# Kernel tuning notes

Measured on AMD Instinct MI355X. Metric: run time of the kernel, lower is better.

Reference implementation:

```python
import jax, jax.numpy as jnp
import numpy as np

M = 12      # max_context_size
H = 768     # hidden_size
NH = 8      # global encoder heads
HD = H // NH
FF = 2048   # global encoder ff_dim
B = 8192


def _gather_hist(buf, mask, idx, ctx):
    """Age-sorted gather of valid circular-buffer slots (oldest first), padded to ctx."""
    Bb, Mx, Hh = buf.shape
    pos = jnp.arange(Mx)
    age = (idx[:, None] - pos[None, :]) % Mx              # [B,M] age of each slot
    key = jnp.where(mask, -age, Mx + 1)                   # valid slots first, oldest (max age) first
    order = jnp.argsort(key, axis=1)                      # stable sort, matches python sorted()
    sorted_buf = jnp.take_along_axis(buf, order[:, :, None], axis=1)
    nvalid = mask.sum(axis=1)                             # [B]
    hist = sorted_buf[:, :ctx]                            # [B,ctx,H]
    valid = jnp.arange(ctx)[None, :] < nvalid[:, None]
    hist = hist * valid[:, :, None]                       # zero out padding rows
    return hist, jnp.minimum(nvalid, ctx)


def _seq_with_current(buf, mask, idx, z_k, ctx):
    """History (ctx-1 slots) + current utterance at the last position (faithful to original,
    including the original's padding-mask behavior arange >= hist_len+1)."""
    Bb = z_k.shape[0]
    hist, hlen = _gather_hist(buf, mask, idx, ctx - 1)
    seq = jnp.concatenate([hist, jnp.zeros((Bb, 1, buf.shape[-1]), buf.dtype)], axis=1)
    seq = seq.at[:, ctx - 1].set(z_k)
    lengths = jnp.minimum(hlen + 1, ctx)
    pad = jnp.arange(ctx)[None, :] >= lengths[:, None]    # True = padded
    return seq, lengths, pad


def _layernorm(x, g, b):
    mu = x.mean(-1, keepdims=True)
    var = x.var(-1, keepdims=True)
    return (x - mu) * jax.lax.rsqrt(var + 1e-5) * g + b


def _forward(z_k, context_buffer, buffer_mask, buffer_indices,
             Wq, bq, Wk, bk, Wv, bv, Wo, bo, ln1_g, ln1_b,
             W1, b1, W2, b2, ln2_g, ln2_b, Wd, bd, Wl, bl, Wg, bg):
    mask = buffer_mask.astype(bool)
    idx = buffer_indices.astype(jnp.int32)
    Bb = z_k.shape[0]

    # ---- global path: 12-slot context -> post-LN transformer layer -> masked mean pool
    gseq, glen, gpad = _seq_with_current(context_buffer, mask, idx, z_k, 12)
    S = 12
    q = (gseq @ Wq + bq).reshape(Bb, S, NH, HD)
    k = (gseq @ Wk + bk).reshape(Bb, S, NH, HD)
    v = (gseq @ Wv + bv).reshape(Bb, S, NH, HD)
    scores = jnp.einsum('bqhd,bkhd->bhqk', q, k) / np.sqrt(HD).astype(np.float32)
    scores = jnp.where(gpad[:, None, None, :], jnp.float32(-1e9), scores)
    attn = jax.nn.softmax(scores, axis=-1)
    ao = jnp.einsum('bhqk,bkhd->bqhd', attn, v).reshape(Bb, S, H) @ Wo + bo
    x = _layernorm(gseq + ao, ln1_g, ln1_b)
    ff = jax.nn.relu(x @ W1 + b1) @ W2 + b2
    x = _layernorm(x + ff, ln2_g, ln2_b)
    gvalid = (~gpad).astype(x.dtype)                       # [B,12]
    denom = jnp.maximum(gvalid.sum(1, keepdims=True), 1.0)
    x_g = (x * gvalid[:, :, None]).sum(1) / denom          # [B,H]

    # ---- direct path
    x_d = jnp.tanh(z_k @ Wd + bd)

    # ---- local path: 5-slot context -> masked mean pool -> projection
    lseq, llen, lpad = _seq_with_current(context_buffer, mask, idx, z_k, 5)
    lvalid = (~lpad).astype(lseq.dtype)
    ldenom = jnp.maximum(lvalid.sum(1, keepdims=True), 1.0)
    lpool = (lseq * lvalid[:, :, None]).sum(1) / ldenom
    x_l = jnp.tanh(lpool @ Wl + bl)

    # ---- gate over [direct, local, global]
    paths = jnp.stack([x_d, x_l, x_g], axis=1)             # [B,3,H]
    logits = paths.reshape(Bb, 3 * H) @ Wg + bg            # [B,3]
    gate = jax.nn.softmax(logits, axis=-1)
    h_k = jnp.einsum('br,brh->bh', gate, paths)
    return h_k


def setup_inputs() -> dict:
    key = jax.random.key(0)
    ks = jax.random.split(key, 24)
    s = 0.02
    inp = {
        'z_k': jax.random.normal(ks[0], (B, H), jnp.float32),
        'context_buffer': jax.random.normal(ks[1], (B, M, H), jnp.float32),
        'buffer_mask': jax.random.randint(ks[2], (B, M), 0, 2, jnp.int32),
        'buffer_indices': jax.random.randint(ks[3], (B,), 0, M, jnp.int32),
        'Wq': jax.random.normal(ks[4], (H, H), jnp.float32) * s,
        'bq': jnp.zeros((H,), jnp.float32),
        'Wk': jax.random.normal(ks[5], (H, H), jnp.float32) * s,
        'bk': jnp.zeros((H,), jnp.float32),
        'Wv': jax.random.normal(ks[6], (H, H), jnp.float32) * s,
        'bv': jnp.zeros((H,), jnp.float32),
        'Wo': jax.random.normal(ks[7], (H, H), jnp.float32) * s,
        'bo': jnp.zeros((H,), jnp.float32),
        'ln1_g': jnp.ones((H,), jnp.float32),
        'ln1_b': jnp.zeros((H,), jnp.float32),
        'W1': jax.random.normal(ks[8], (H, FF), jnp.float32) * s,
        'b1': jnp.zeros((FF,), jnp.float32),
        'W2': jax.random.normal(ks[9], (FF, H), jnp.float32) * s,
        'b2': jnp.zeros((H,), jnp.float32),
        'ln2_g': jnp.ones((H,), jnp.float32),
        'ln2_b': jnp.zeros((H,), jnp.float32),
        'Wd': jax.random.normal(ks[10], (H, H), jnp.float32) * s,
        'bd': jnp.zeros((H,), jnp.float32),
        'Wl': jax.random.normal(ks[11], (H, H), jnp.float32) * s,
        'bl': jnp.zeros((H,), jnp.float32),
        'Wg': jax.random.normal(ks[12], (3 * H, 3), jnp.float32) * s,
        'bg': jnp.zeros((3,), jnp.float32),
    }
    return inp


def reference(z_k, context_buffer, buffer_mask, buffer_indices,
              Wq, bq, Wk, bk, Wv, bv, Wo, bo, ln1_g, ln1_b,
              W1, b1, W2, b2, ln2_g, ln2_b, Wd, bd, Wl, bl, Wg, bg):
    return _forward(z_k, context_buffer, buffer_mask, buffer_indices,
                    Wq, bq, Wk, bk, Wv, bv, Wo, bo, ln1_g, ln1_b,
                    W1, b1, W2, b2, ln2_g, ln2_b, Wd, bd, Wl, bl, Wg, bg)
```

## Files before the change

### kernel.cpp

```cpp
#include <hip/hip_runtime.h>
#include <cstdint>
#include <cstddef>

typedef __bf16 bf16;
typedef __attribute__((ext_vector_type(8))) __bf16 bf16x8;
typedef __attribute__((ext_vector_type(4))) float f32x4;

#define B_TOT 8192

__device__ __forceinline__ void gload16(const void* g, void* l) {
  __builtin_amdgcn_global_load_lds(
      (__attribute__((address_space(1))) void*)g,
      (__attribute__((address_space(3))) void*)l, 16, 0, 0);
}

__device__ __forceinline__ void block_sum2(float& a, float& b, float* lds8) {
#pragma unroll
  for (int o = 32; o; o >>= 1) {
    a += __shfl_xor(a, o, 64);
    b += __shfl_xor(b, o, 64);
  }
  int w = threadIdx.x >> 6;
  if ((threadIdx.x & 63) == 0) { lds8[w] = a; lds8[4 + w] = b; }
  __syncthreads();
  a = lds8[0] + lds8[1] + lds8[2] + lds8[3];
  b = lds8[4] + lds8[5] + lds8[6] + lds8[7];
  __syncthreads();
}

__global__ __launch_bounds__(256) void scan1_kernel(
    const int* __restrict__ mask, int* __restrict__ Lg, int* __restrict__ lbase,
    int* __restrict__ btot, int b0)
{
  __shared__ int ts[256];
  const int t = threadIdx.x;
  const int b = blockIdx.x * 256 + t;
  const int* mp = mask + (long)(b0 + b) * 12;
  int nv = 0;
#pragma unroll
  for (int p = 0; p < 12; ++p) nv += (mp[p] != 0);
  int L = (nv < 11 ? nv : 11) + 1;
  ts[t] = L;
  __syncthreads();
  for (int o = 1; o < 256; o <<= 1) {
    int v = (t >= o) ? ts[t - o] : 0;
    __syncthreads();
    ts[t] += v;
    __syncthreads();
  }
  Lg[b] = L;
  lbase[b] = ts[t] - L;
  if (t == 255) btot[blockIdx.x] = ts[255];
}

__global__ __launch_bounds__(64) void scan2_kernel(
    const int* __restrict__ btot, int* __restrict__ boff, int* __restrict__ meta, int nb)
{
  if (threadIdx.x == 0) {
    int acc = 0;
    for (int i = 0; i < nb; ++i) { int v = btot[i]; boff[i] = acc; acc += v; }
    meta[0] = acc;
  }
}

__global__ __launch_bounds__(256) void prep_kernel(
    const float* __restrict__ z, const float* __restrict__ buf,
    const int* __restrict__ mask, const int* __restrict__ idxs,
    const int* __restrict__ lbase, const int* __restrict__ boff,
    int* __restrict__ fbase, bf16* __restrict__ gseq,
    bf16* __restrict__ zl, int b0, int Bc)
{
  const int bl = blockIdx.x;
  const int b  = b0 + bl;
  __shared__ int ord[12];
  __shared__ int s_nv;
  if (threadIdx.x == 0) {
    int id = idxs[b];
    int nv = 0;
    for (int a = 11; a >= 0; --a) {
      int pos = id - a; if (pos < 0) pos += 12;
      if (mask[b * 12 + pos]) ord[nv++] = pos;
    }
    s_nv = nv;
  }
  const long bs = (long)lbase[bl] + boff[bl >> 8];
  if (threadIdx.x == 0) fbase[bl] = (int)bs;
  __syncthreads();
  const int nv = s_nv;
  const int hg = (nv < 11 ? nv : 11);
  const int hl = (nv < 4 ? nv : 4);
  const float ld = 1.0f / (float)(hl + 1);
  for (int c = threadIdx.x; c < 768; c += 256) {
    float zv = z[(long)b * 768 + c];
    zl[(long)bl * 768 + c] = (bf16)zv;
    float ls = 0.0f;
    for (int s = 0; s < hg; ++s) {
      float v = buf[((long)b * 12 + ord[s]) * 768 + c];
      gseq[(bs + s) * 768 + c] = (bf16)v;
      if (s < hl) ls += v;
    }
    gseq[(bs + hg) * 768 + c] = (hg == 11) ? (bf16)zv : (bf16)0.0f;
    if (nv >= 4) ls += zv;
    zl[((long)Bc + bl) * 768 + c] = (bf16)(ls * ld);
  }
}

__global__ __launch_bounds__(256) void transpose_bf16(
    const float* __restrict__ W, bf16* __restrict__ Wt, int K, int N)
{
  __shared__ float tile[32][33];
  int bn = blockIdx.x * 32;
  int bk = blockIdx.y * 32;
  int tx = threadIdx.x & 31;
  int ty0 = threadIdx.x >> 5;
  for (int ty = ty0; ty < 32; ty += 8)
    tile[ty][tx] = W[(long)(bk + ty) * N + bn + tx];
  __syncthreads();
  for (int ty = ty0; ty < 32; ty += 8)
    Wt[(long)(bn + ty) * K + bk + tx] = (bf16)tile[tx][ty];
}

__global__ __launch_bounds__(256) void pack3_kernel(
    const float* __restrict__ a, const float* __restrict__ b,
    const float* __restrict__ c, float* __restrict__ out)
{
  int t = blockIdx.x * blockDim.x + threadIdx.x;
  if (t < 768) out[t] = a[t];
  else if (t < 1536) out[t] = b[t - 768];
  else if (t < 2304) out[t] = c[t - 1536];
}

__global__ __launch_bounds__(256, 2) void gemm_bt(
    const bf16* __restrict__ A, const bf16* __restrict__ Bt,
    const float* __restrict__ bias, void* __restrict__ C,
    int K, int N, int act, int outf32,
    const int* __restrict__ mlim, int msplit,
    const bf16* __restrict__ Bt2, const float* __restrict__ bias2)
{
  __shared__ __align__(16) bf16 smem[2 * 128 * 64];
  bf16* As = smem;
  bf16* Bs = smem + 128 * 64;
  int gx = gridDim.x, gy = gridDim.y;
  int bx = blockIdx.x, by = blockIdx.y;
  if ((gy & 7) == 0) {
    int l = bx + gx * by;
    int xcd = l & 7, slot = l >> 3;
    bx = slot % gx;
    by = (slot / gx) * 8 + xcd;
  }
  const long m0 = (long)by * 128;
  const long n0 = (long)bx * 128;
  if (mlim && m0 >= mlim[0]) return;
  const bf16* Bsel = (m0 >= msplit) ? Bt2 : Bt;
  const float* bsel = (m0 >= msplit) ? bias2 : bias;

  const int tid  = threadIdx.x;
  const int wave = tid >> 6;
  const int lane = tid & 63;
  const int wm = (wave >> 1) * 64;
  const int wn = (wave & 1) * 64;
  const int i16  = lane & 15;
  const int quad = lane >> 4;
  const int l8 = lane >> 3;
  const int c7 = lane & 7;

  const int csrc = c7 ^ l8;
  const bf16* Ag[4]; const bf16* Bg[4];
  bf16* Al[4]; bf16* Bl[4];
#pragma unroll
  for (int u = 0; u < 4; ++u) {
    int r = wave * 32 + u * 8 + l8;
    Ag[u] = A    + (m0 + r) * K + csrc * 8;
    Bg[u] = Bsel + (n0 + r) * K + csrc * 8;
    Al[u] = As + (wave * 32 + u * 8) * 64 + lane * 8;
    Bl[u] = Bs + (wave * 32 + u * 8) * 64 + lane * 8;
  }

  f32x4 acc[4][4] = {};

  for (int kt = 0; kt < K; kt += 64) {
    __syncthreads();
#pragma unroll
    for (int u = 0; u < 4; ++u) {
      gload16(Ag[u] + kt, Al[u]);
      gload16(Bg[u] + kt, Bl[u]);
    }
    __syncthreads();
#pragma unroll
    for (int s = 0; s < 2; ++s) {
      const int cofs = ((s << 2) | quad) ^ c7;
      bf16x8 af[4], bfr[4];
#pragma unroll
      for (int i = 0; i < 4; ++i)
        af[i] = *(const bf16x8*)(As + (wm + i * 16 + i16) * 64 + cofs * 8);
#pragma unroll
      for (int j = 0; j < 4; ++j)
        bfr[j] = *(const bf16x8*)(Bs + (wn + j * 16 + i16) * 64 + cofs * 8);
#pragma unroll
      for (int i = 0; i < 4; ++i)
#pragma unroll
        for (int j = 0; j < 4; ++j)
          acc[i][j] = __builtin_amdgcn_mfma_f32_16x16x32_bf16(af[i], bfr[j], acc[i][j], 0, 0, 0);
    }
  }

  if (!outf32) {
    __syncthreads();
    bf16* Cs = smem;
#pragma unroll
    for (int j = 0; j < 4; ++j) {
      int col = wn + j * 16 + i16;
      int c8s = (col >> 3) ^ (quad << 1);
      int clo = col & 7;
      float bv = bsel[n0 + col];
#pragma unroll
      for (int i = 0; i < 4; ++i) {
#pragma unroll
        for (int r = 0; r < 4; ++r) {
          int row = wm + i * 16 + quad * 4 + r;
          float v = acc[i][j][r] + bv;
          if (act == 1) v = fmaxf(v, 0.0f);
          Cs[row * 128 + c8s * 8 + clo] = (bf16)v;
        }
      }
    }
    __syncthreads();
    bf16* Cg = (bf16*)C;
#pragma unroll
    for (int u = 0; u < 8; ++u) {
      int g = u * 256 + tid;
      int row = g >> 4, c8 = g & 15;
      int c8s = c8 ^ (((row >> 2) & 3) << 1);
      *(bf16x8*)(Cg + (m0 + row) * N + n0 + c8 * 8) =
          *(const bf16x8*)(Cs + row * 128 + c8s * 8);
    }
  } else {
#pragma unroll
    for (int i = 0; i < 4; ++i) {
#pragma unroll
      for (int j = 0; j < 4; ++j) {
        long col = n0 + wn + j * 16 + i16;
        float bv = bsel[col];
#pragma unroll
        for (int r = 0; r < 4; ++r) {
          long row = m0 + wm + i * 16 + quad * 4 + r;
          float v = acc[i][j][r] + bv;
          if (act == 1) v = fmaxf(v, 0.0f);
          else if (act == 2) v = tanhf(v);
          ((float*)C)[row * N + col] = v;
        }
      }
    }
  }
}

__global__ __launch_bounds__(256) void attn_kernel(
    const bf16* __restrict__ QKV, const int* __restrict__ fbase,
    const int* __restrict__ Lg, bf16* __restrict__ AO)
{
  const int bl  = blockIdx.x;
  const int tid = threadIdx.x;
  const int L   = Lg[bl];
  const long bs = fbase[bl];
  const bf16* qb = QKV + bs * 2304;
  __shared__ bf16 kx[12 * 776];
  __shared__ bf16 vx[12 * 776];
  __shared__ float att[8][12][12];
  const int LH = L * 768;
  for (int t = tid; t < LH; t += 256) {
    int s = t / 768, c = t - s * 768;
    kx[s * 776 + c] = qb[(long)s * 2304 + 768 + c];
    vx[s * 776 + c] = qb[(long)s * 2304 + 1536 + c];
  }
  __syncthreads();
  const int LL = L * L;
  for (int t = tid; t < 8 * LL; t += 256) {
    int h = t / LL, r = t - h * LL, i = r / L, j = r - (r / L) * L;
    const bf16x8* q = (const bf16x8*)(qb + (long)i * 2304 + h * 96);
    const bf16x8* k = (const bf16x8*)(kx + j * 776 + h * 96);
    float a = 0.0f;
#pragma unroll
    for (int d = 0; d < 12; ++d) {
      bf16x8 qa = q[d], ka = k[d];
#pragma unroll
      for (int e = 0; e < 8; ++e) a += (float)qa[e] * (float)ka[e];
    }
    att[h][i][j] = a * 0.10206207261596575f;
  }
  __syncthreads();
  for (int t = tid; t < 8 * L; t += 256) {
    int h = t / L, i = t - (t / L) * L;
    float mx = -3e38f;
    for (int j = 0; j < L; ++j) mx = fmaxf(mx, att[h][i][j]);
    float sum = 0.0f;
    for (int j = 0; j < L; ++j) { float e = __expf(att[h][i][j] - mx); att[h][i][j] = e; sum += e; }
    float inv = 1.0f / sum;
    for (int j = 0; j < L; ++j) att[h][i][j] *= inv;
  }
  __syncthreads();
  for (int t = tid; t < LH; t += 256) {
    int i = t / 768, c = t - i * 768, h = c / 96;
    float a = 0.0f;
    for (int j = 0; j < L; ++j) a += att[h][i][j] * (float)vx[j * 776 + c];
    AO[(bs + i) * 768 + c] = (bf16)a;
  }
}

__global__ __launch_bounds__(256) void ln1_kernel(
    const bf16* __restrict__ WoO, const bf16* __restrict__ gseq,
    const float* __restrict__ gam, const float* __restrict__ bet,
    bf16* __restrict__ X, const int* __restrict__ meta)
{
  const long row = blockIdx.x;
  if (row >= meta[0]) return;
  const int tid = threadIdx.x;
  __shared__ float red[8];
  float v[3]; float s = 0.0f, ss = 0.0f;
#pragma unroll
  for (int u = 0; u < 3; ++u) {
    int c = tid + u * 256;
    float x = (float)WoO[row * 768 + c] + (float)gseq[row * 768 + c];
    v[u] = x; s += x; ss += x * x;
  }
  block_sum2(s, ss, red);
  float mu  = s * (1.0f / 768.0f);
  float var = ss * (1.0f / 768.0f) - mu * mu;
  float inv = 1.0f / sqrtf(var + 1e-5f);
#pragma unroll
  for (int u = 0; u < 3; ++u) {
    int c = tid + u * 256;
    X[row * 768 + c] = (bf16)((v[u] - mu) * inv * gam[c] + bet[c]);
  }
}

__global__ __launch_bounds__(256) void ln2gate_kernel(
    const bf16* __restrict__ X, const bf16* __restrict__ FFo,
    const float* __restrict__ gam, const float* __restrict__ bet,
    const int* __restrict__ fbase, const int* __restrict__ Lg,
    const float* __restrict__ xdl, const float* __restrict__ Wg,
    const float* __restrict__ bg, float* __restrict__ out, int b0, int Bc)
{
  const int bl = blockIdx.x;
  const int tid = threadIdx.x;
  const int L = Lg[bl];
  const long bs = fbase[bl];
  __shared__ float red[8];
  __shared__ float red3[12];
  float p0 = 0.0f, p1 = 0.0f, p2 = 0.0f;
  for (int s = 0; s < L; ++s) {
    long row = bs + s;
    float v[3]; float sm = 0.0f, sq = 0.0f;
#pragma unroll
    for (int u = 0; u < 3; ++u) {
      int c = tid + u * 256;
      float x = (float)X[row * 768 + c] + (float)FFo[row * 768 + c];
      v[u] = x; sm += x; sq += x * x;
    }
    block_sum2(sm, sq, red);
    float mu  = sm * (1.0f / 768.0f);
    float var = sq * (1.0f / 768.0f) - mu * mu;
    float inv = 1.0f / sqrtf(var + 1e-5f);
    p0 += (v[0] - mu) * inv * gam[tid]       + bet[tid];
    p1 += (v[1] - mu) * inv * gam[tid + 256] + bet[tid + 256];
    p2 += (v[2] - mu) * inv * gam[tid + 512] + bet[tid + 512];
  }
  float dn = 1.0f / (float)L;
  p0 *= dn; p1 *= dn; p2 *= dn;
  const float* xd = xdl + (long)bl * 768;
  const float* xl = xdl + ((long)Bc + bl) * 768;
  float xd0 = xd[tid], xd1 = xd[tid + 256], xd2 = xd[tid + 512];
  float xl0 = xl[tid], xl1 = xl[tid + 256], xl2 = xl[tid + 512];
  float l0 = 0.0f, l1 = 0.0f, l2 = 0.0f;
#pragma unroll
  for (int r = 0; r < 3; ++r) {
    float lr = xd0 * Wg[tid * 3 + r] + xd1 * Wg[(tid + 256) * 3 + r] + xd2 * Wg[(tid + 512) * 3 + r]
             + xl0 * Wg[(768 + tid) * 3 + r] + xl1 * Wg[(1024 + tid) * 3 + r] + xl2 * Wg[(1280 + tid) * 3 + r]
             + p0 * Wg[(1536 + tid) * 3 + r] + p1 * Wg[(1792 + tid) * 3 + r] + p2 * Wg[(2048 + tid) * 3 + r];
    if (r == 0) l0 = lr; else if (r == 1) l1 = lr; else l2 = lr;
  }
#pragma unroll
  for (int o = 32; o; o >>= 1) {
    l0 += __shfl_xor(l0, o, 64);
    l1 += __shfl_xor(l1, o, 64);
    l2 += __shfl_xor(l2, o, 64);
  }
  if ((tid & 63) == 0) { int w = tid >> 6; red3[w * 3] = l0; red3[w * 3 + 1] = l1; red3[w * 3 + 2] = l2; }
  __syncthreads();
  l0 = red3[0] + red3[3] + red3[6] + red3[9]  + bg[0];
  l1 = red3[1] + red3[4] + red3[7] + red3[10] + bg[1];
  l2 = red3[2] + red3[5] + red3[8] + red3[11] + bg[2];
  float mx = fmaxf(l0, fmaxf(l1, l2));
  float e0 = __expf(l0 - mx), e1 = __expf(l1 - mx), e2 = __expf(l2 - mx);
  float inv = 1.0f / (e0 + e1 + e2);
  e0 *= inv; e1 *= inv; e2 *= inv;
  float* op = out + (long)(b0 + bl) * 768;
  op[tid]       = e0 * xd0 + e1 * xl0 + e2 * p0;
  op[tid + 256] = e0 * xd1 + e1 * xl1 + e2 * p1;
  op[tid + 512] = e0 * xd2 + e1 * xl2 + e2 * p2;
}

extern "C" void kernel_launch(void* const* d_in, const int* in_sizes, int n_in,
                              void* d_out, int out_size, void* d_ws, size_t ws_size,
                              hipStream_t stream) {
  const float* z    = (const float*)d_in[0];
  const float* buf  = (const float*)d_in[1];
  const int*   mask = (const int*)d_in[2];
  const int*   idxs = (const int*)d_in[3];
  const float* Wq = (const float*)d_in[4];  const float* bq = (const float*)d_in[5];
  const float* Wk = (const float*)d_in[6];  const float* bk = (const float*)d_in[7];
  const float* Wv = (const float*)d_in[8];  const float* bv = (const float*)d_in[9];
  const float* Wo = (const float*)d_in[10]; const float* bo = (const float*)d_in[11];
  const float* ln1g = (const float*)d_in[12]; const float* ln1b = (const float*)d_in[13];
  const float* W1 = (const float*)d_in[14]; const float* b1 = (const float*)d_in[15];
  const float* W2 = (const float*)d_in[16]; const float* b2 = (const float*)d_in[17];
  const float* ln2g = (const float*)d_in[18]; const float* ln2b = (const float*)d_in[19];
  const float* Wd = (const float*)d_in[20]; const float* bd = (const float*)d_in[21];
  const float* Wl = (const float*)d_in[22]; const float* blw = (const float*)d_in[23];
  const float* Wg = (const float*)d_in[24]; const float* bg = (const float*)d_in[25];
  float* out = (float*)d_out;
  (void)in_sizes; (void)n_in; (void)out_size;

  auto rnd = [](size_t x) { return (x + 255) & ~(size_t)255; };

  size_t fixed = 0;
  fixed += rnd((size_t)2304 * 768 * 2);
  fixed += rnd((size_t)768 * 768 * 2);
  fixed += rnd((size_t)2048 * 768 * 2);
  fixed += rnd((size_t)768 * 2048 * 2);
  fixed += rnd((size_t)768 * 768 * 2) * 2;
  fixed += rnd((size_t)2304 * 4) + 256 + 512 + 512;

  auto chunkBytes = [&](size_t bc) {
    return rnd((size_t)55296 * bc) + 3 * rnd((size_t)18432 * bc)
         + rnd((size_t)3072 * bc) + rnd((size_t)6144 * bc)
         + 3 * rnd((size_t)4 * bc);
  };
  int Bc = 8192;
  while (Bc > 1024 && fixed + chunkBytes(Bc) > ws_size) Bc >>= 1;

  size_t off = 0;
  auto alloc = [&](size_t n) { void* p = (char*)d_ws + off; off += rnd(n); return p; };
  bf16* Wqkv_t = (bf16*)alloc((size_t)2304 * 768 * 2);
  bf16* Wo_t   = (bf16*)alloc((size_t)768 * 768 * 2);
  bf16* W1_t   = (bf16*)alloc((size_t)2048 * 768 * 2);
  bf16* W2_t   = (bf16*)alloc((size_t)768 * 2048 * 2);
  bf16* Wd_t   = (bf16*)alloc((size_t)768 * 768 * 2);
  bf16* Wl_t   = (bf16*)alloc((size_t)768 * 768 * 2);
  float* bqkv  = (float*)alloc((size_t)2304 * 4);
  int*  meta   = (int*)alloc(256);
  int*  btot   = (int*)alloc(512);
  int*  boff   = (int*)alloc(512);
  bf16* P1 = (bf16*)alloc((size_t)55296 * Bc);
  bf16* P2 = (bf16*)alloc((size_t)18432 * Bc);
  bf16* P3 = (bf16*)alloc((size_t)18432 * Bc);
  bf16* P4 = (bf16*)alloc((size_t)18432 * Bc);
  bf16* zl   = (bf16*)alloc((size_t)3072 * Bc);
  float* xdl = (float*)alloc((size_t)6144 * Bc);
  int*  Lg    = (int*)alloc((size_t)4 * Bc);
  int*  lbase = (int*)alloc((size_t)4 * Bc);
  int*  fbase = (int*)alloc((size_t)4 * Bc);

  transpose_bf16<<<dim3(24, 24), 256, 0, stream>>>(Wq, Wqkv_t,                 768, 768);
  transpose_bf16<<<dim3(24, 24), 256, 0, stream>>>(Wk, Wqkv_t + 768 * 768,     768, 768);
  transpose_bf16<<<dim3(24, 24), 256, 0, stream>>>(Wv, Wqkv_t + 2 * 768 * 768, 768, 768);
  transpose_bf16<<<dim3(24, 24), 256, 0, stream>>>(Wo, Wo_t, 768, 768);
  transpose_bf16<<<dim3(64, 24), 256, 0, stream>>>(W1, W1_t, 768, 2048);
  transpose_bf16<<<dim3(24, 64), 256, 0, stream>>>(W2, W2_t, 2048, 768);
  transpose_bf16<<<dim3(24, 24), 256, 0, stream>>>(Wd, Wd_t, 768, 768);
  transpose_bf16<<<dim3(24, 24), 256, 0, stream>>>(Wl, Wl_t, 768, 768);
  pack3_kernel<<<9, 256, 0, stream>>>(bq, bk, bv, bqkv);

  const int BIG = 0x7fffffff;
  for (int b0 = 0; b0 < B_TOT; b0 += Bc) {
    const int Ycap = (12 * Bc) / 128;
    scan1_kernel<<<Bc / 256, 256, 0, stream>>>(mask, Lg, lbase, btot, b0);
    scan2_kernel<<<1, 64, 0, stream>>>(btot, boff, meta, Bc / 256);
    prep_kernel<<<Bc, 256, 0, stream>>>(z, buf, mask, idxs, lbase, boff, fbase, P2, zl, b0, Bc);
    gemm_bt<<<dim3(6, (2 * Bc) / 128), 256, 0, stream>>>(zl, Wd_t, bd, xdl, 768, 768, 2, 1, nullptr, Bc, Wl_t, blw);
    gemm_bt<<<dim3(18, Ycap), 256, 0, stream>>>(P2, Wqkv_t, bqkv, P1, 768, 2304, 0, 0, meta, BIG, nullptr, nullptr);
    attn_kernel<<<Bc, 256, 0, stream>>>(P1, fbase, Lg, P3);
    gemm_bt<<<dim3(6, Ycap), 256, 0, stream>>>(P3, Wo_t, bo, P4, 768, 768, 0, 0, meta, BIG, nullptr, nullptr);
    ln1_kernel<<<12 * Bc, 256, 0, stream>>>(P4, P2, ln1g, ln1b, P3, meta);
    gemm_bt<<<dim3(16, Ycap), 256, 0, stream>>>(P3, W1_t, b1, P1, 768, 2048, 1, 0, meta, BIG, nullptr, nullptr);
    gemm_bt<<<dim3(6, Ycap), 256, 0, stream>>>(P1, W2_t, b2, P2, 2048, 768, 0, 0, meta, BIG, nullptr, nullptr);
    ln2gate_kernel<<<Bc, 256, 0, stream>>>(P3, P2, ln2g, ln2b, fbase, Lg, xdl, Wg, bg, out, b0, Bc);
  }
}
```

Baseline: 1.594 ms.

## Vectorize attention kernel loads, swizzle K in LDS, read V directly from global

The attention kernel now stages only K into shared memory, using 16-byte vector copies and an XOR swizzle in place of row padding to avoid bank conflicts. The P·V stage reads V straight from global memory in bf16x8 vectors and writes eight outputs per thread. It also sets an occupancy hint of 8 blocks per SM in launch_bounds. Together these cut LDS usage and scalar memory traffic, at the cost of more global reads of V through the cache and possible register pressure from the occupancy hint.

```diff
diff --git a/kernel.cpp b/kernel.cpp
--- a/kernel.cpp
+++ b/kernel.cpp
@@ -254,7 +254,7 @@
   }
 }
 
-__global__ __launch_bounds__(256) void attn_kernel(
+__global__ __launch_bounds__(256, 8) void attn_kernel(
     const bf16* __restrict__ QKV, const int* __restrict__ fbase,
     const int* __restrict__ Lg, bf16* __restrict__ AO)
 {
@@ -263,25 +263,27 @@
   const int L   = Lg[bl];
   const long bs = fbase[bl];
   const bf16* qb = QKV + bs * 2304;
-  __shared__ bf16 kx[12 * 776];
-  __shared__ bf16 vx[12 * 776];
+  __shared__ bf16 kx[12 * 768];
   __shared__ float att[8][12][12];
-  const int LH = L * 768;
-  for (int t = tid; t < LH; t += 256) {
-    int s = t / 768, c = t - s * 768;
-    kx[s * 776 + c] = qb[(long)s * 2304 + 768 + c];
-    vx[s * 776 + c] = qb[(long)s * 2304 + 1536 + c];
+  const int LC = L * 96;
+  for (int t = tid; t < LC; t += 256) {
+    int s = t / 96, c8 = t - s * 96;
+    *(bf16x8*)(kx + s * 768 + ((c8 ^ (s & 7)) << 3)) =
+        *(const bf16x8*)(qb + (long)s * 2304 + 768 + (c8 << 3));
   }
   __syncthreads();
   const int LL = L * L;
   for (int t = tid; t < 8 * LL; t += 256) {
     int h = t / LL, r = t - h * LL, i = r / L, j = r - (r / L) * L;
     const bf16x8* q = (const bf16x8*)(qb + (long)i * 2304 + h * 96);
-    const bf16x8* k = (const bf16x8*)(kx + j * 776 + h * 96);
+    const bf16* kr = kx + j * 768;
+    const int cb = h * 12;
+    const int jx = j & 7;
     float a = 0.0f;
 #pragma unroll
     for (int d = 0; d < 12; ++d) {
-      bf16x8 qa = q[d], ka = k[d];
+      bf16x8 qa = q[d];
+      bf16x8 ka = *(const bf16x8*)(kr + (((cb + d) ^ jx) << 3));
 #pragma unroll
       for (int e = 0; e < 8; ++e) a += (float)qa[e] * (float)ka[e];
     }
@@ -298,11 +300,21 @@
     for (int j = 0; j < L; ++j) att[h][i][j] *= inv;
   }
   __syncthreads();
-  for (int t = tid; t < LH; t += 256) {
-    int i = t / 768, c = t - i * 768, h = c / 96;
-    float a = 0.0f;
-    for (int j = 0; j < L; ++j) a += att[h][i][j] * (float)vx[j * 776 + c];
-    AO[(bs + i) * 768 + c] = (bf16)a;
+  for (int t = tid; t < LC; t += 256) {
+    int i = t / 96, c8 = t - i * 96;
+    int h = c8 / 12;
+    const bf16* vp = qb + 1536 + (c8 << 3);
+    float acc[8] = {};
+    for (int j = 0; j < L; ++j) {
+      float a = att[h][i][j];
+      bf16x8 vv = *(const bf16x8*)(vp + (long)j * 2304);
+#pragma unroll
+      for (int e = 0; e < 8; ++e) acc[e] += a * (float)vv[e];
+    }
+    bf16x8 o;
+#pragma unroll
+    for (int e = 0; e < 8; ++e) o[e] = (bf16)acc[e];
+    *(bf16x8*)(AO + (bs + i) * 768 + (c8 << 3)) = o;
   }
 }
 
```

After: 1.499 ms. 6.0% less time.
